# Kernel tuning notes

Measured on AMD Instinct MI355X. Metric: run time of the kernel, lower is better.

## Reference

```python
import jax, jax.numpy as jnp
import numpy as np

EMBED = 1024
ADIM = 1024
H = 16
HD = ADIM // H          # 64
RAY = 48                # ray_subdim
R = RAY // 3            # 16
SCALE = 1.0 / np.sqrt(HD)
NB = 768                # boundary tokens
MN = 8                  # max neighbors
FG = 6                  # face_group
L = 1024                # tokens per face
B = 12                  # b * face_group
STAGES = 4


def _apply_dray(x, d, einsum_str, inverse):
    ray = x[..., :RAY].reshape(x.shape[:-1] + (3, R))
    if inverse:
        d = jnp.swapaxes(d, -1, -2)
    ray = jnp.einsum(einsum_str, d, ray).reshape(x.shape[:-1] + (RAY,))
    return jnp.concatenate([ray, x[..., RAY:]], axis=-1)


def setup_inputs() -> dict:
    key = jax.random.key(0)
    ks = jax.random.split(key, 12)
    inp = {}
    inp['x'] = jax.random.normal(ks[0], (B, L, EMBED), dtype=jnp.float32)
    inp['qkv_w'] = jax.random.normal(ks[1], (EMBED, 3 * ADIM), dtype=jnp.float32) * 0.02
    inp['out_w'] = jax.random.normal(ks[2], (ADIM, EMBED), dtype=jnp.float32) * 0.02
    inp['out_b'] = jax.random.normal(ks[3], (EMBED,), dtype=jnp.float32) * 0.02
    inp['d_ray'] = jax.random.normal(ks[4], (STAGES, FG, L, 3, 3), dtype=jnp.float32)
    inp['boundary_face_ids'] = jax.random.randint(ks[5], (NB,), 0, FG, dtype=jnp.int32).astype(jnp.int64)
    inp['boundary_token_indices'] = jnp.arange(NB, dtype=jnp.int64)
    inp['boundary_local_indices'] = jax.random.randint(ks[6], (NB,), 0, L, dtype=jnp.int32).astype(jnp.int64)
    inp['boundary_stage_ids'] = jax.random.randint(ks[7], (NB,), 0, STAGES, dtype=jnp.int32).astype(jnp.int64)
    inp['neighbor_face_ids'] = jax.random.randint(ks[8], (NB, MN), 0, FG, dtype=jnp.int32).astype(jnp.int64)
    inp['neighbor_token_indices'] = jax.random.randint(ks[9], (NB, MN), 0, L, dtype=jnp.int32).astype(jnp.int64)
    inp['neighbor_local_indices'] = jax.random.randint(ks[10], (NB, MN), 0, L, dtype=jnp.int32).astype(jnp.int64)
    inp['neighbor_stage_ids'] = jax.random.randint(ks[11], (NB, MN), 0, STAGES, dtype=jnp.int32).astype(jnp.int64)
    inp['neighbor_mask'] = jnp.ones((NB, MN), dtype=bool)
    inp['face_group'] = FG
    return inp


def reference(x, qkv_w, out_w, out_b, d_ray,
              boundary_face_ids, boundary_token_indices, boundary_local_indices, boundary_stage_ids,
              neighbor_face_ids, neighbor_token_indices, neighbor_local_indices, neighbor_stage_ids,
              neighbor_mask, face_group):
    b = x.shape[0] // face_group
    l = x.shape[1]
    xt = x.reshape(b, face_group, l, EMBED)          # [b, FG, L, E]
    max_face, max_idx = face_group - 1, l - 1

    qf = jnp.clip(boundary_face_ids, 0, max_face)
    qi = jnp.clip(boundary_token_indices, 0, max_idx)
    valid_q = (boundary_face_ids == qf) & (boundary_token_indices == qi)

    nf = jnp.clip(neighbor_face_ids, 0, max_face)
    ni = jnp.clip(neighbor_token_indices, 0, max_idx)
    mask = neighbor_mask & (neighbor_face_ids == nf) & (neighbor_token_indices == ni)

    # gather boundary queries and neighbor keys/values
    x_q = xt[:, qf, qi, :]                            # [b, NB, E]
    x_kv = xt[:, nf, ni, :]                           # [b, NB, MN, E]
    q = (x_q @ qkv_w)[..., :ADIM]
    kv = x_kv @ qkv_w
    k = kv[..., ADIM:2 * ADIM]
    v = kv[..., 2 * ADIM:]

    nb, mn = q.shape[1], k.shape[2]
    q = q.reshape(b, nb, H, HD)
    k = k.reshape(b, nb, mn, H, HD)
    v = v.reshape(b, nb, mn, H, HD)

    d_q = d_ray[boundary_stage_ids, boundary_face_ids, boundary_local_indices]     # [NB, 3, 3]
    d_k = d_ray[neighbor_stage_ids,
                jnp.maximum(neighbor_face_ids, 0),
                jnp.maximum(neighbor_local_indices, 0)]                            # [NB, MN, 3, 3]

    q = _apply_dray(q, d_q, 'nij,bnhjr->bnhir', inverse=False)
    k = _apply_dray(k, d_k, 'nmij,bnmhjr->bnmhir', inverse=False)
    v = _apply_dray(v, d_k, 'nmij,bnmhjr->bnmhir', inverse=False)

    attn = jnp.einsum('bnhd,bnmhd->bnmh', q, k) * SCALE
    attn = jnp.where(mask[None, :, :, None], attn, -jnp.inf)
    attn = jax.nn.softmax(attn, axis=2)               # softmax over neighbors
    out = jnp.einsum('bnmh,bnmhd->bnhd', attn, v)

    out = _apply_dray(out, d_q, 'nij,bnhjr->bnhir', inverse=True)
    out = out.reshape(b, nb, ADIM) @ out_w + out_b
    out = out * valid_q[None, :, None].astype(out.dtype)

    out_full = jnp.zeros_like(xt).at[:, qf, qi, :].set(out)
    return out_full.reshape(-1, l, EMBED)
```

## Files before the change

### kernel.cpp

```cpp
#include <hip/hip_runtime.h>
#include <hip/hip_bf16.h>
#include <cstddef>

#define FG 6
#define L 1024
#define NB 768
#define MN 8
#define H 16
#define HD 64
#define ADIM 1024
#define STAGES 4
#define SCALE 0.125f

typedef __attribute__((ext_vector_type(8))) short bf16x8;
typedef __attribute__((ext_vector_type(4))) float f32x4;
typedef __attribute__((address_space(3))) short lds_short_t;
typedef const __attribute__((address_space(1))) short g_short_t;

__device__ __forceinline__ int clampi(int v, int lo, int hi) {
  return v < lo ? lo : (v > hi ? hi : v);
}

__device__ __forceinline__ short f2bf(float f) {
  __hip_bfloat16 h = __float2bfloat16(f);
  return *reinterpret_cast<short*>(&h);
}

__device__ __forceinline__ void gload16(const short* g, short* l) {
  __builtin_amdgcn_global_load_lds((g_short_t*)g, (lds_short_t*)l, 16, 0, 0);
}

__global__ __launch_bounds__(256)
void conv_bf16(const float* __restrict__ in, short* __restrict__ out) {
  size_t i = ((size_t)blockIdx.x * 256 + threadIdx.x) * 8;
  float4 a = *(const float4*)(in + i);
  float4 b = *(const float4*)(in + i + 4);
  bf16x8 v;
  v[0] = f2bf(a.x); v[1] = f2bf(a.y); v[2] = f2bf(a.z); v[3] = f2bf(a.w);
  v[4] = f2bf(b.x); v[5] = f2bf(b.y); v[6] = f2bf(b.z); v[7] = f2bf(b.w);
  *(bf16x8*)(out + i) = v;
}

__global__ __launch_bounds__(256)
void transpose_conv(const float* __restrict__ in, short* __restrict__ out,
                    int K, int N) {
  __shared__ float tile[32][33];
  const int n0 = blockIdx.x * 32, k0 = blockIdx.y * 32;
  const int tx = threadIdx.x & 31, ty = threadIdx.x >> 5;
  #pragma unroll
  for (int i = 0; i < 4; ++i)
    tile[ty + i * 8][tx] = in[(size_t)(k0 + ty + i * 8) * N + n0 + tx];
  __syncthreads();
  #pragma unroll
  for (int i = 0; i < 4; ++i)
    out[(size_t)(n0 + ty + i * 8) * K + k0 + tx] =
        f2bf(tile[tx][ty + i * 8]);
}

template<int MODE>
__global__ __launch_bounds__(256)
void mfma_gemm(const short* __restrict__ A, const short* __restrict__ B,
               void* __restrict__ Cv,
               const int* __restrict__ f_ids, const int* __restrict__ t_ids,
               const float* __restrict__ bias)
{
  constexpr int KT    = 16;
  constexpr int BCOL0 = (MODE == 1) ? 1024 : 0;

  __shared__ __align__(16) short As[8192];
  __shared__ __align__(16) short Bs[8192];

  const int tid  = threadIdx.x;
  const int w    = tid >> 6, lane = tid & 63;
  const int row0 = blockIdx.y * 128, col0 = blockIdx.x * 128;

  size_t aoff[4], boff[4];
  short *adst[4], *bdst[4];
  #pragma unroll
  for (int c = 0; c < 4; ++c) {
    const int d = (w * 4 + c) * 64 + lane;
    const int r = d >> 3;
    const int ssrc = (d & 7) ^ (r & 7);
    long gr;
    if (MODE == 2) {
      gr = row0 + r;
    } else {
      const int rr = row0 + r;
      int bi, idx;
      if (MODE == 0) { bi = rr >= NB;          idx = rr - bi * NB; }
      else           { bi = rr >= NB * MN;     idx = rr - bi * NB * MN; }
      const int f = clampi(f_ids[idx], 0, FG - 1);
      const int q = clampi(t_ids[idx], 0, L - 1);
      gr = (long)(bi * FG + f) * L + q;
    }
    aoff[c] = (size_t)gr * 1024 + ssrc * 8;
    boff[c] = (size_t)(BCOL0 + col0 + r) * 1024 + ssrc * 8;
    adst[c] = As + (w * 4 + c) * 512;
    bdst[c] = Bs + (w * 4 + c) * 512;
  }

  const int lr = lane & 15, lq = lane >> 4;
  const int wrow = (w >> 1) * 64, wcol = (w & 1) * 64;
  const int sA = lr & 7;
  const char* As8 = (const char*)As;
  const char* Bs8 = (const char*)Bs;
  const int abase = (wrow + lr) * 128;
  const int bbase = (wcol + lr) * 128;

  f32x4 acc[4][4];
  #pragma unroll
  for (int m = 0; m < 4; ++m)
    #pragma unroll
    for (int n = 0; n < 4; ++n) acc[m][n] = (f32x4){0.f, 0.f, 0.f, 0.f};

  for (int kt = 0; kt < KT; ++kt) {
    #pragma unroll
    for (int c = 0; c < 4; ++c) {
      gload16(A + aoff[c] + kt * 64, adst[c]);
      gload16(B + boff[c] + kt * 64, bdst[c]);
    }
    __syncthreads();
    #pragma unroll
    for (int kk = 0; kk < 2; ++kk) {
      const int so = ((kk * 4 + lq) ^ sA) << 4;
      bf16x8 av[4], bv[4];
      #pragma unroll
      for (int m = 0; m < 4; ++m)
        av[m] = *(const bf16x8*)(As8 + abase + m * 2048 + so);
      #pragma unroll
      for (int n = 0; n < 4; ++n)
        bv[n] = *(const bf16x8*)(Bs8 + bbase + n * 2048 + so);
      #pragma unroll
      for (int m = 0; m < 4; ++m)
        #pragma unroll
        for (int n = 0; n < 4; ++n)
          acc[m][n] = __builtin_amdgcn_mfma_f32_16x16x32_bf16(
              av[m], bv[n], acc[m][n], 0, 0, 0);
    }
    __syncthreads();
  }

  if (MODE == 0) {
    float* C = (float*)Cv;
    #pragma unroll
    for (int m = 0; m < 4; ++m)
      #pragma unroll
      for (int j = 0; j < 4; ++j) {
        const int r = row0 + wrow + m * 16 + lq * 4 + j;
        #pragma unroll
        for (int n = 0; n < 4; ++n)
          C[(size_t)r * 1024 + col0 + wcol + n * 16 + lr] = acc[m][n][j];
      }
  } else if (MODE == 1) {
    short* C = (short*)Cv;
    #pragma unroll
    for (int m = 0; m < 4; ++m)
      #pragma unroll
      for (int j = 0; j < 4; ++j) {
        const int r = row0 + wrow + m * 16 + lq * 4 + j;
        #pragma unroll
        for (int n = 0; n < 4; ++n)
          C[(size_t)r * 2048 + col0 + wcol + n * 16 + lr] = f2bf(acc[m][n][j]);
      }
  } else {
    float* C = (float*)Cv;
    float bb[4];
    #pragma unroll
    for (int n = 0; n < 4; ++n) bb[n] = bias[col0 + wcol + n * 16 + lr];
    #pragma unroll
    for (int m = 0; m < 4; ++m)
      #pragma unroll
      for (int j = 0; j < 4; ++j) {
        const int r  = row0 + wrow + m * 16 + lq * 4 + j;
        const int bi = r >= NB;
        const int nn = r - bi * NB;
        const int bf = f_ids[nn], bt = t_ids[nn];
        const int qf = clampi(bf, 0, FG - 1), qi = clampi(bt, 0, L - 1);
        const bool valid = (bf == qf) && (bt == qi);
        const size_t obase = ((size_t)(bi * FG + qf) * L + qi) * 1024;
        #pragma unroll
        for (int n = 0; n < 4; ++n) {
          const int col = col0 + wcol + n * 16 + lr;
          C[obase + col] = valid ? (acc[m][n][j] + bb[n]) : 0.f;
        }
      }
  }
}

__global__ __launch_bounds__(256)
void attn_kernel(const float* __restrict__ dray,
                 const int* __restrict__ bfid, const int* __restrict__ blid,
                 const int* __restrict__ bsid,
                 const int* __restrict__ nfid, const int* __restrict__ ntid,
                 const int* __restrict__ nlid, const int* __restrict__ nsid,
                 const int* __restrict__ nmask,
                 const float* __restrict__ qbuf,
                 const __hip_bfloat16* __restrict__ kvbuf,
                 __hip_bfloat16* __restrict__ obuf)
{
  const int lane = threadIdx.x & 63;
  const int gw   = blockIdx.x * 4 + (threadIdx.x >> 6);
  const int h    = gw & (H - 1);
  const int bn   = gw >> 4;
  const int n    = bn % NB;

  int st = clampi(bsid[n], 0, STAGES - 1);
  int f  = clampi(bfid[n], 0, FG - 1);
  int lc = clampi(blid[n], 0, L - 1);
  const float* dqp = dray + ((size_t)(st * FG + f) * L + lc) * 9;
  float dq[9];
  #pragma unroll
  for (int t = 0; t < 9; ++t) dq[t] = dqp[t];

  const float qraw = qbuf[(size_t)bn * ADIM + h * HD + lane];
  const int rr = lane & 15;

  float x0 = __shfl(qraw, rr), x1 = __shfl(qraw, 16 + rr), x2 = __shfl(qraw, 32 + rr);
  float q0 = dq[0]*x0 + dq[1]*x1 + dq[2]*x2;
  float q1 = dq[3]*x0 + dq[4]*x1 + dq[5]*x2;
  float q2 = dq[6]*x0 + dq[7]*x1 + dq[8]*x2;
  float qd = lane < 16 ? q0 : lane < 32 ? q1 : lane < 48 ? q2 : qraw;

  const __hip_bfloat16* kvb = kvbuf + (size_t)bn * MN * 2048 + h * HD;
  float s[MN], vd[MN];
  #pragma unroll
  for (int m = 0; m < MN; ++m) {
    const int idx = n * MN + m;
    int nst = clampi(nsid[idx], 0, STAGES - 1);
    int nfc = clampi(nfid[idx], 0, FG - 1);
    int nlc = clampi(nlid[idx], 0, L - 1);
    const float* dkp = dray + ((size_t)(nst * FG + nfc) * L + nlc) * 9;
    float dk[9];
    #pragma unroll
    for (int t = 0; t < 9; ++t) dk[t] = dkp[t];

    float kraw = __bfloat162float(kvb[(size_t)m * 2048 + lane]);
    float k0 = __shfl(kraw, rr), k1 = __shfl(kraw, 16 + rr), k2 = __shfl(kraw, 32 + rr);
    float kr0 = dk[0]*k0 + dk[1]*k1 + dk[2]*k2;
    float kr1 = dk[3]*k0 + dk[4]*k1 + dk[5]*k2;
    float kr2 = dk[6]*k0 + dk[7]*k1 + dk[8]*k2;
    float kd = lane < 16 ? kr0 : lane < 32 ? kr1 : lane < 48 ? kr2 : kraw;

    float p = qd * kd;
    #pragma unroll
    for (int off = 32; off; off >>= 1) p += __shfl_xor(p, off);
    s[m] = p;

    float vraw = __bfloat162float(kvb[(size_t)m * 2048 + 1024 + lane]);
    float v0 = __shfl(vraw, rr), v1 = __shfl(vraw, 16 + rr), v2 = __shfl(vraw, 32 + rr);
    float vr0 = dk[0]*v0 + dk[1]*v1 + dk[2]*v2;
    float vr1 = dk[3]*v0 + dk[4]*v1 + dk[5]*v2;
    float vr2 = dk[6]*v0 + dk[7]*v1 + dk[8]*v2;
    vd[m] = lane < 16 ? vr0 : lane < 32 ? vr1 : lane < 48 ? vr2 : vraw;
  }

  float mx = -INFINITY;
  #pragma unroll
  for (int m = 0; m < MN; ++m) {
    const int idx = n * MN + m;
    int nf = nfid[idx], nt = ntid[idx];
    bool ok = (nmask[idx] != 0) && nf >= 0 && nf < FG && nt >= 0 && nt < L;
    s[m] = ok ? s[m] * SCALE : -INFINITY;
    mx = fmaxf(mx, s[m]);
  }
  float den = 0.f;
  #pragma unroll
  for (int m = 0; m < MN; ++m) { s[m] = expf(s[m] - mx); den += s[m]; }
  float inv = 1.0f / den;

  float od = 0.f;
  #pragma unroll
  for (int m = 0; m < MN; ++m) od += s[m] * vd[m];
  od *= inv;

  float y0 = __shfl(od, rr), y1 = __shfl(od, 16 + rr), y2 = __shfl(od, 32 + rr);
  float t0 = dq[0]*y0 + dq[3]*y1 + dq[6]*y2;
  float t1 = dq[1]*y0 + dq[4]*y1 + dq[7]*y2;
  float t2 = dq[2]*y0 + dq[5]*y1 + dq[8]*y2;
  float outd = lane < 16 ? t0 : lane < 32 ? t1 : lane < 48 ? t2 : od;

  obuf[(size_t)bn * ADIM + h * HD + lane] = __float2bfloat16(outd);
}

extern "C" void kernel_launch(void* const* d_in, const int* in_sizes, int n_in,
                              void* d_out, int out_size, void* d_ws, size_t ws_size,
                              hipStream_t stream) {
  const float* x     = (const float*)d_in[0];
  const float* qkv_w = (const float*)d_in[1];
  const float* out_w = (const float*)d_in[2];
  const float* out_b = (const float*)d_in[3];
  const float* dray  = (const float*)d_in[4];
  const int* bfid  = (const int*)d_in[5];
  const int* btid  = (const int*)d_in[6];
  const int* blid  = (const int*)d_in[7];
  const int* bsid  = (const int*)d_in[8];
  const int* nfid  = (const int*)d_in[9];
  const int* ntid  = (const int*)d_in[10];
  const int* nlid  = (const int*)d_in[11];
  const int* nsid  = (const int*)d_in[12];
  const int* nmask = (const int*)d_in[13];

  char* ws = (char*)d_ws;
  short* xb    = (short*)(ws);
  short* qwT   = (short*)(ws + 25165824);
  short* owT   = (short*)(ws + 31457280);
  float* qbuf  = (float*)(ws + 33554432);
  short* kvbuf = (short*)(ws + 39845888);
  short* obuf  = (short*)(ws + 90177536);

  hipMemsetAsync(d_out, 0, (size_t)out_size * sizeof(float), stream);

  conv_bf16<<<6144, 256, 0, stream>>>(x, xb);
  transpose_conv<<<dim3(96, 32), 256, 0, stream>>>(qkv_w, qwT, 1024, 3072);
  transpose_conv<<<dim3(32, 32), 256, 0, stream>>>(out_w, owT, 1024, 1024);

  mfma_gemm<0><<<dim3(8, 12), 256, 0, stream>>>(xb, qwT, qbuf, bfid, btid, nullptr);
  mfma_gemm<1><<<dim3(16, 96), 256, 0, stream>>>(xb, qwT, kvbuf, nfid, ntid, nullptr);
  attn_kernel<<<6144, 256, 0, stream>>>(dray, bfid, blid, bsid,
                                        nfid, ntid, nlid, nsid, nmask,
                                        qbuf, (const __hip_bfloat16*)kvbuf,
                                        (__hip_bfloat16*)obuf);
  mfma_gemm<2><<<dim3(8, 12), 256, 0, stream>>>(obuf, owT, d_out, bfid, btid, out_b);
}
```

Before: 183.4 us.

## Replace KV gather GEMM with 256x256-tile eight-wave pipelined MFMA kernel

Adds a dedicated KV projection GEMM that uses 256x256 output tiles with 512 threads. Gathered A rows and weight rows are staged into swizzled, double-buffered LDS with async global loads, and the loop is hand-scheduled with barriers, explicit waitcnts and setprio around MFMA bursts. The goal is to raise MFMA utilization and operand reuse over the previous generic 128-tile GEMM, and to hide global load latency. In exchange it uses 128KB of LDS per block, a large accumulator register footprint, and a fragile manual schedule whose vmcnt counts must exactly match the issued loads.

```diff
diff --git a/kernel.cpp b/kernel.cpp
--- a/kernel.cpp
+++ b/kernel.cpp
@@ -187,6 +187,194 @@
   }
 }
 
+
+#define BAR()   do { __builtin_amdgcn_s_barrier(); __builtin_amdgcn_sched_barrier(0); } while (0)
+#define LGKM0() do { asm volatile("s_waitcnt lgkmcnt(0)" ::: "memory"); __builtin_amdgcn_sched_barrier(0); } while (0)
+#define VMC(N)  do { asm volatile("s_waitcnt vmcnt(" #N ")" ::: "memory"); __builtin_amdgcn_sched_barrier(0); } while (0)
+#define PRIO1   __builtin_amdgcn_s_setprio(1)
+#define PRIO0   __builtin_amdgcn_s_setprio(0)
+
+#define LDA(D, FB, KK, BUF)                                                   \
+  { _Pragma("unroll")                                                         \
+    for (int f_ = 0; f_ < 4; ++f_) {                                          \
+      const int row_ = (2 * ((FB) + f_) + wm) * 16 + lr;                      \
+      D[f_] = *(const bf16x8*)(As8 + (BUF) * 32768 + ((FB) >= 4 ? 16384 : 0)  \
+               + (row_ & 127) * 128 + ((((KK) * 4 + lq) ^ aswz) << 4));       \
+    } }
+
+#define LDB(D, KK, BUF)                                                       \
+  { _Pragma("unroll")                                                         \
+    for (int g_ = 0; g_ < 4; ++g_) {                                          \
+      const int row_ = wn * 64 + g_ * 16 + lr;                                \
+      D[g_] = *(const bf16x8*)(Bs8 + (BUF) * 32768 + (KK) * 16384             \
+               + row_ * 64 + ((lq ^ bswz) << 4));                             \
+    } }
+
+#define MM(AV, BV, FB)                                                        \
+  { _Pragma("unroll")                                                         \
+    for (int f_ = 0; f_ < 4; ++f_)                                            \
+      _Pragma("unroll")                                                       \
+      for (int g_ = 0; g_ < 4; ++g_)                                          \
+        acc[(FB) + f_][g_] = __builtin_amdgcn_mfma_f32_16x16x32_bf16(         \
+            AV[f_], BV[g_], acc[(FB) + f_][g_], 0, 0, 0); }
+
+__global__ __launch_bounds__(512, 2)
+void kv_gemm8(const short* __restrict__ A, const short* __restrict__ B,
+              short* __restrict__ C,
+              const int* __restrict__ f_ids, const int* __restrict__ t_ids)
+{
+  __shared__ __align__(16) short As[32768];
+  __shared__ __align__(16) short Bs[32768];
+
+  const int tid = threadIdx.x;
+  const int w = tid >> 6, lane = tid & 63;
+  const int wm = w >> 2, wn = w & 3;
+  const int lr = lane & 15, lq = lane >> 4;
+  const int row0 = blockIdx.y * 256;
+  const int col0 = blockIdx.x * 256;
+
+  int aoff[2][2];
+  const int sA = ((lane & 7) ^ (lane >> 3)) * 8;
+  #pragma unroll
+  for (int h = 0; h < 2; ++h)
+    #pragma unroll
+    for (int c = 0; c < 2; ++c) {
+      const int tr = h * 128 + w * 16 + c * 8 + (lane >> 3);
+      const int rr = row0 + tr;
+      const int bi = rr >= NB * MN;
+      const int idx = rr - bi * (NB * MN);
+      const int f = clampi(f_ids[idx], 0, FG - 1);
+      const int q = clampi(t_ids[idx], 0, L - 1);
+      aoff[h][c] = ((bi * FG + f) * L + q) * 1024 + sA;
+    }
+  int boff[2][2];
+  const int sB = ((lane & 3) ^ ((lane >> 2) & 3)) * 8;
+  #pragma unroll
+  for (int h = 0; h < 2; ++h)
+    #pragma unroll
+    for (int c = 0; c < 2; ++c) {
+      const int br = w * 32 + c * 16 + (lane >> 2);
+      boff[h][c] = (1024 + col0 + br) * 1024 + h * 32 + sB;
+    }
+
+  auto stgA = [&](int h, int kt, int buf) {
+    gload16(A + aoff[h][0] + kt * 64, As + buf * 16384 + h * 8192 + (w * 2 + 0) * 512);
+    gload16(A + aoff[h][1] + kt * 64, As + buf * 16384 + h * 8192 + (w * 2 + 1) * 512);
+  };
+  auto stgB = [&](int h, int kt, int buf) {
+    gload16(B + boff[h][0] + kt * 64, Bs + buf * 16384 + h * 8192 + (w * 2 + 0) * 512);
+    gload16(B + boff[h][1] + kt * 64, Bs + buf * 16384 + h * 8192 + (w * 2 + 1) * 512);
+  };
+
+  const char* As8 = (const char*)As;
+  const char* Bs8 = (const char*)Bs;
+  const int aswz = lr & 7;
+  const int bswz = lr & 3;
+
+  f32x4 acc[8][4];
+  #pragma unroll
+  for (int f = 0; f < 8; ++f)
+    #pragma unroll
+    for (int g = 0; g < 4; ++g) acc[f][g] = (f32x4){0.f, 0.f, 0.f, 0.f};
+
+  bf16x8 av[4], bv0[4], bv1[4];
+
+  stgB(0, 0, 0); stgB(1, 0, 0); stgA(0, 0, 0); stgA(1, 0, 0);
+  stgB(0, 1, 1); stgB(1, 1, 1); stgA(0, 1, 1);
+  VMC(8); BAR();
+
+  for (int I = 0; I < 7; ++I) {
+    const int t1 = 2 * I + 1, t2 = 2 * I + 2, t3 = 2 * I + 3;
+    LDA(av, 0, 0, 0); LDB(bv0, 0, 0);
+    stgA(1, t1, 1);
+    BAR(); LGKM0();
+    PRIO1; MM(av, bv0, 0); PRIO0;
+    BAR();
+    LDA(av, 0, 1, 0); LDB(bv1, 1, 0);
+    stgB(0, t2, 0);
+    BAR(); LGKM0();
+    PRIO1; MM(av, bv1, 0); PRIO0;
+    VMC(10); BAR();
+    LDA(av, 4, 0, 0);
+    stgB(1, t2, 0);
+    BAR(); LGKM0();
+    PRIO1; MM(av, bv0, 4); PRIO0;
+    BAR();
+    LDA(av, 4, 1, 0);
+    stgA(0, t2, 0);
+    BAR(); LGKM0();
+    PRIO1; MM(av, bv1, 4); PRIO0;
+    VMC(8); BAR();
+    LDA(av, 0, 0, 1); LDB(bv0, 0, 1);
+    stgA(1, t2, 0);
+    BAR(); LGKM0();
+    PRIO1; MM(av, bv0, 0); PRIO0;
+    BAR();
+    LDA(av, 0, 1, 1); LDB(bv1, 1, 1);
+    stgB(0, t3, 1);
+    BAR(); LGKM0();
+    PRIO1; MM(av, bv1, 0); PRIO0;
+    VMC(10); BAR();
+    LDA(av, 4, 0, 1);
+    stgB(1, t3, 1);
+    BAR(); LGKM0();
+    PRIO1; MM(av, bv0, 4); PRIO0;
+    BAR();
+    LDA(av, 4, 1, 1);
+    stgA(0, t3, 1);
+    BAR(); LGKM0();
+    PRIO1; MM(av, bv1, 4); PRIO0;
+    VMC(8); BAR();
+  }
+
+  {
+    LDA(av, 0, 0, 0); LDB(bv0, 0, 0);
+    stgA(1, 15, 1);
+    BAR(); LGKM0();
+    PRIO1; MM(av, bv0, 0); PRIO0;
+    BAR();
+    LDA(av, 0, 1, 0); LDB(bv1, 1, 0);
+    BAR(); LGKM0();
+    PRIO1; MM(av, bv1, 0); PRIO0;
+    VMC(8); BAR();
+    LDA(av, 4, 0, 0);
+    BAR(); LGKM0();
+    PRIO1; MM(av, bv0, 4); PRIO0;
+    BAR();
+    LDA(av, 4, 1, 0);
+    BAR(); LGKM0();
+    PRIO1; MM(av, bv1, 4); PRIO0;
+    VMC(2); BAR();
+    LDA(av, 0, 0, 1); LDB(bv0, 0, 1);
+    BAR(); LGKM0();
+    PRIO1; MM(av, bv0, 0); PRIO0;
+    BAR();
+    LDA(av, 0, 1, 1); LDB(bv1, 1, 1);
+    BAR(); LGKM0();
+    PRIO1; MM(av, bv1, 0); PRIO0;
+    VMC(0); BAR();
+    LDA(av, 4, 0, 1);
+    BAR(); LGKM0();
+    PRIO1; MM(av, bv0, 4); PRIO0;
+    BAR();
+    LDA(av, 4, 1, 1);
+    LGKM0();
+    PRIO1; MM(av, bv1, 4); PRIO0;
+  }
+
+  #pragma unroll
+  for (int f = 0; f < 8; ++f) {
+    #pragma unroll
+    for (int j = 0; j < 4; ++j) {
+      const int r = row0 + (2 * f + wm) * 16 + lq * 4 + j;
+      short* cp = C + (size_t)r * 2048 + col0 + wn * 64 + lr;
+      #pragma unroll
+      for (int g = 0; g < 4; ++g)
+        cp[g * 16] = f2bf(acc[f][g][j]);
+    }
+  }
+}
+
 __global__ __launch_bounds__(256)
 void attn_kernel(const float* __restrict__ dray,
                  const int* __restrict__ bfid, const int* __restrict__ blid,
@@ -315,7 +503,7 @@
   transpose_conv<<<dim3(32, 32), 256, 0, stream>>>(out_w, owT, 1024, 1024);
 
   mfma_gemm<0><<<dim3(8, 12), 256, 0, stream>>>(xb, qwT, qbuf, bfid, btid, nullptr);
-  mfma_gemm<1><<<dim3(16, 96), 256, 0, stream>>>(xb, qwT, kvbuf, nfid, ntid, nullptr);
+  kv_gemm8<<<dim3(8, 48), 512, 0, stream>>>(xb, qwT, kvbuf, nfid, ntid);
   attn_kernel<<<6144, 256, 0, stream>>>(dray, bfid, blid, bsid,
                                         nfid, ntid, nlid, nsid, nmask,
                                         qbuf, (const __hip_bfloat16*)kvbuf,
```

Result: no change. 184.9 us (+0.8%).

## Replace KV gather GEMM with 192x256 tile, 8-wave software-pipelined kernel

Applied to the files above, without the earlier changes.

Swaps the generic 128x128 MFMA GEMM used for the gathered K/V projection for a dedicated kernel with 192x256 tiles, 512 threads, double-buffered LDS with XOR swizzle, and an explicitly scheduled interleave of global loads, LDS reads and MFMA. It uses manual waitcnt, barriers and setprio. The goal is to hide load latency behind MFMA and raise data reuse per block, cutting the dominant GEMM's time. The cost is fragile hand scheduling, heavy register and LDS use (112KB LDS per block with 2 blocks per CU), and fewer blocks (512), which may under-fill the GPU.

```diff
diff --git a/kernel.cpp b/kernel.cpp
--- a/kernel.cpp
+++ b/kernel.cpp
@@ -151,17 +151,6 @@
         for (int n = 0; n < 4; ++n)
           C[(size_t)r * 1024 + col0 + wcol + n * 16 + lr] = acc[m][n][j];
       }
-  } else if (MODE == 1) {
-    short* C = (short*)Cv;
-    #pragma unroll
-    for (int m = 0; m < 4; ++m)
-      #pragma unroll
-      for (int j = 0; j < 4; ++j) {
-        const int r = row0 + wrow + m * 16 + lq * 4 + j;
-        #pragma unroll
-        for (int n = 0; n < 4; ++n)
-          C[(size_t)r * 2048 + col0 + wcol + n * 16 + lr] = f2bf(acc[m][n][j]);
-      }
   } else {
     float* C = (float*)Cv;
     float bb[4];
@@ -184,6 +173,170 @@
           C[obase + col] = valid ? (acc[m][n][j] + bb[n]) : 0.f;
         }
       }
+  }
+}
+
+
+#define BAR()   do { __builtin_amdgcn_s_barrier(); __builtin_amdgcn_sched_barrier(0); } while (0)
+#define LGKM(N) do { asm volatile("s_waitcnt lgkmcnt(" #N ")" ::: "memory"); __builtin_amdgcn_sched_barrier(0); } while (0)
+#define VMC(N)  do { asm volatile("s_waitcnt vmcnt(" #N ")" ::: "memory"); __builtin_amdgcn_sched_barrier(0); } while (0)
+#define PRIO1   __builtin_amdgcn_s_setprio(1)
+#define PRIO0   __builtin_amdgcn_s_setprio(0)
+
+#define LDA6(D, FB, KK, BUF)                                                  \
+  { _Pragma("unroll")                                                         \
+    for (int f_ = 0; f_ < 3; ++f_) {                                          \
+      const int row_ = (2 * ((FB) + f_) + wm) * 16 + lr;                      \
+      D[f_] = *(const bf16x8*)(As8 + (BUF) * 24576 + row_ * 128               \
+               + ((((KK) * 4 + lq) ^ swz) << 4));                             \
+    } }
+
+#define LDB4(D, KK, BUF)                                                      \
+  { _Pragma("unroll")                                                         \
+    for (int g_ = 0; g_ < 4; ++g_) {                                          \
+      const int row_ = wn * 64 + g_ * 16 + lr;                                \
+      D[g_] = *(const bf16x8*)(Bs8 + (BUF) * 32768 + row_ * 128               \
+               + ((((KK) * 4 + lq) ^ swz) << 4));                             \
+    } }
+
+#define MM6(AV, BV, FB)                                                       \
+  { _Pragma("unroll")                                                         \
+    for (int f_ = 0; f_ < 3; ++f_)                                            \
+      _Pragma("unroll")                                                       \
+      for (int g_ = 0; g_ < 4; ++g_)                                          \
+        acc[(FB) + f_][g_] = __builtin_amdgcn_mfma_f32_16x16x32_bf16(         \
+            AV[f_], BV[g_], acc[(FB) + f_][g_], 0, 0, 0); }
+
+__global__ __launch_bounds__(512, 2)
+void kv_gemm192(const short* __restrict__ A, const short* __restrict__ B,
+                short* __restrict__ C,
+                const int* __restrict__ f_ids, const int* __restrict__ t_ids)
+{
+  __shared__ __align__(16) short As[24576];
+  __shared__ __align__(16) short Bs[32768];
+
+  const int tid = threadIdx.x;
+  const int w = tid >> 6, lane = tid & 63;
+  const int wm = w >> 2, wn = w & 3;
+  const int lr = lane & 15, lq = lane >> 4;
+  const int row0 = blockIdx.y * 192;
+  const int col0 = blockIdx.x * 256;
+
+  const int ssrc = (((tid & 7) ^ ((tid >> 3) & 7))) * 8;
+
+  size_t a_src[3];
+  #pragma unroll
+  for (int c = 0; c < 3; ++c) {
+    const int rr = row0 + c * 64 + (tid >> 3);
+    const int bi = rr >= NB * MN;
+    const int idx = rr - bi * (NB * MN);
+    const int f = clampi(f_ids[idx], 0, FG - 1);
+    const int q = clampi(t_ids[idx], 0, L - 1);
+    a_src[c] = (size_t)((bi * FG + f) * L + q) * 1024 + ssrc;
+  }
+  size_t b_src[2][2];
+  #pragma unroll
+  for (int h = 0; h < 2; ++h)
+    #pragma unroll
+    for (int i = 0; i < 2; ++i)
+      b_src[h][i] = (size_t)(1024 + col0 + h * 128 + ((tid + i * 512) >> 3)) * 1024 + ssrc;
+
+  auto stgA = [&](int c, int kt, int buf) {
+    gload16(A + a_src[c] + kt * 64, As + buf * 12288 + c * 4096 + tid * 8);
+  };
+  auto stgB = [&](int h, int kt, int buf) {
+    gload16(B + b_src[h][0] + kt * 64, Bs + buf * 16384 + h * 8192 + tid * 8);
+    gload16(B + b_src[h][1] + kt * 64, Bs + buf * 16384 + h * 8192 + 4096 + tid * 8);
+  };
+
+  const char* As8 = (const char*)As;
+  const char* Bs8 = (const char*)Bs;
+  const int swz = lane & 7;
+
+  f32x4 acc[6][4];
+  #pragma unroll
+  for (int f = 0; f < 6; ++f)
+    #pragma unroll
+    for (int g = 0; g < 4; ++g) acc[f][g] = (f32x4){0.f, 0.f, 0.f, 0.f};
+
+  bf16x8 avA[3], avB[3], bv0[4], bv1[4];
+
+  stgB(0, 0, 0); stgB(1, 0, 0); stgA(0, 0, 0); stgA(1, 0, 0); stgA(2, 0, 0);
+  stgB(0, 1, 1); stgB(1, 1, 1); stgA(0, 1, 1);
+  VMC(5); BAR();
+  LDA6(avA, 0, 0, 0); LDB4(bv0, 0, 0);
+
+  for (int I = 0; I < 7; ++I) {
+    const int kA = 2 * I + 1, kB = 2 * I + 2, kC = 2 * I + 3;
+    BAR(); stgA(1, kA, 1);
+    LDA6(avB, 0, 1, 0); LDB4(bv1, 1, 0);
+    LGKM(7); PRIO1; MM6(avA, bv0, 0); PRIO0;
+    BAR(); stgA(2, kA, 1);
+    LDA6(avA, 3, 0, 0);
+    LGKM(3); PRIO1; MM6(avB, bv1, 0); PRIO0;
+    BAR(); stgB(0, kB, 0); VMC(2);
+    LDA6(avB, 3, 1, 0);
+    LGKM(3); PRIO1; MM6(avA, bv0, 3); PRIO0;
+    BAR(); stgB(1, kB, 0); stgA(0, kB, 0);
+    LDA6(avA, 0, 0, 1); LDB4(bv0, 0, 1);
+    LGKM(7); PRIO1; MM6(avB, bv1, 3); PRIO0;
+    BAR(); stgA(1, kB, 0);
+    LDA6(avB, 0, 1, 1); LDB4(bv1, 1, 1);
+    LGKM(7); PRIO1; MM6(avA, bv0, 0); PRIO0;
+    BAR(); stgA(2, kB, 0);
+    LDA6(avA, 3, 0, 1);
+    LGKM(3); PRIO1; MM6(avB, bv1, 0); PRIO0;
+    BAR(); stgB(0, kC, 1); VMC(2);
+    LDA6(avB, 3, 1, 1);
+    LGKM(3); PRIO1; MM6(avA, bv0, 3); PRIO0;
+    BAR(); stgB(1, kC, 1); stgA(0, kC, 1);
+    LDA6(avA, 0, 0, 0); LDB4(bv0, 0, 0);
+    LGKM(7); PRIO1; MM6(avB, bv1, 3); PRIO0;
+  }
+
+  {
+    BAR(); stgA(1, 15, 1);
+    LDA6(avB, 0, 1, 0); LDB4(bv1, 1, 0);
+    LGKM(7); PRIO1; MM6(avA, bv0, 0); PRIO0;
+
+    BAR(); stgA(2, 15, 1);
+    LDA6(avA, 3, 0, 0);
+    LGKM(3); PRIO1; MM6(avB, bv1, 0); PRIO0;
+
+    BAR(); VMC(0);
+    LDA6(avB, 3, 1, 0);
+    LGKM(3); PRIO1; MM6(avA, bv0, 3); PRIO0;
+
+    BAR();
+    LDA6(avA, 0, 0, 1); LDB4(bv0, 0, 1);
+    LGKM(7); PRIO1; MM6(avB, bv1, 3); PRIO0;
+
+    BAR();
+    LDA6(avB, 0, 1, 1); LDB4(bv1, 1, 1);
+    LGKM(7); PRIO1; MM6(avA, bv0, 0); PRIO0;
+
+    BAR();
+    LDA6(avA, 3, 0, 1);
+    LGKM(3); PRIO1; MM6(avB, bv1, 0); PRIO0;
+
+    BAR();
+    LDA6(avB, 3, 1, 1);
+    LGKM(3); PRIO1; MM6(avA, bv0, 3); PRIO0;
+
+    BAR();
+    LGKM(0); PRIO1; MM6(avB, bv1, 3); PRIO0;
+  }
+
+  #pragma unroll
+  for (int f = 0; f < 6; ++f) {
+    #pragma unroll
+    for (int j = 0; j < 4; ++j) {
+      const int r = row0 + (2 * f + wm) * 16 + lq * 4 + j;
+      short* cp = C + (size_t)r * 2048 + col0 + wn * 64 + lr;
+      #pragma unroll
+      for (int g = 0; g < 4; ++g)
+        cp[g * 16] = f2bf(acc[f][g][j]);
+    }
   }
 }
 
@@ -315,7 +468,7 @@
   transpose_conv<<<dim3(32, 32), 256, 0, stream>>>(out_w, owT, 1024, 1024);
 
   mfma_gemm<0><<<dim3(8, 12), 256, 0, stream>>>(xb, qwT, qbuf, bfid, btid, nullptr);
-  mfma_gemm<1><<<dim3(16, 96), 256, 0, stream>>>(xb, qwT, kvbuf, nfid, ntid, nullptr);
+  kv_gemm192<<<dim3(8, 64), 512, 0, stream>>>(xb, qwT, kvbuf, nfid, ntid);
   attn_kernel<<<6144, 256, 0, stream>>>(dray, bfid, blid, bsid,
                                         nfid, ntid, nlid, nsid, nmask,
                                         qbuf, (const __hip_bfloat16*)kvbuf,
```

Result: no change. 181.0 us (-1.3%).
